# Performance work log

Hardware: AMD Instinct MI355X
Metric: run time of the kernel (lower is better)

The kernel has to match this reference:

```python
import jax, jax.numpy as jnp
import numpy as np

B, F, N = 16, 128, 20000  # batch, feature (edge==node==message size), num nodes
M = F  # message_size = edge_feature_size


def setup_inputs() -> dict:
    key = jax.random.key(0)
    ks = jax.random.split(key, 9)
    s = 1.0 / np.sqrt(F)
    return {
        "h_w": jax.random.normal(ks[0], (B, F, N), jnp.float32),
        "h_v": jax.random.normal(ks[1], (B, F), jnp.float32),
        "e_wv": jax.random.normal(ks[2], (B, F, N), jnp.float32),
        "W_e2m": jax.random.normal(ks[3], (M, F), jnp.float32) * s,
        "b_e2m": jax.random.normal(ks[4], (M,), jnp.float32) * s,
        "W_n2m": jax.random.normal(ks[5], (M, F), jnp.float32) * s,
        "b_n2m": jax.random.normal(ks[6], (M,), jnp.float32) * s,
        "W_resize": jax.random.normal(ks[7], (M, 3 * M), jnp.float32) * (1.0 / np.sqrt(3 * M)),
        "b_resize": jax.random.normal(ks[8], (M,), jnp.float32) * (1.0 / np.sqrt(3 * M)),
    }


def reference(h_w, h_v, e_wv, W_e2m, b_e2m, W_n2m, b_n2m, W_resize, b_resize):
    # Per-node loop vectorized over the node axis n.
    # tmp_msg = cat([e2m(e_wv[:,:,n]), n2m(h_w[:,:,n]), n2m(h_v)], dim=1)
    # message[:,:,n] = resize_m(tmp_msg)
    # Split W_resize into its three column blocks to avoid materializing the
    # [B, 3M, N] concat: resize(cat(a,b,c)) = Wa@a + Wb@b + Wc@c + b.
    Wa = W_resize[:, :M]          # acts on e2m output
    Wb = W_resize[:, M:2 * M]     # acts on n2m(h_w)
    Wc = W_resize[:, 2 * M:]      # acts on n2m(h_v)

    em = jnp.einsum('bfn,mf->bmn', e_wv, W_e2m) + b_e2m[:, None]   # [B,M,N]
    nw = jnp.einsum('bfn,mf->bmn', h_w, W_n2m) + b_n2m[:, None]    # [B,M,N]
    nv = h_v @ W_n2m.T + b_n2m                                      # [B,M]

    msg = (jnp.einsum('bmn,km->bkn', em, Wa)
           + jnp.einsum('bmn,km->bkn', nw, Wb)
           + ((nv @ Wc.T) + b_resize)[:, :, None])                  # [B,M,N]
    return msg
```

## Files before the change

kernel.cpp:

```cpp
#include <hip/hip_runtime.h>
#include <hip/hip_bf16.h>

typedef __attribute__((ext_vector_type(8))) short bf16x8;
typedef __attribute__((ext_vector_type(4))) float f32x4;

#define B_DIM 16
#define F_DIM 128
#define N_DIM 20000
#define M_DIM 128
#define NW 32
#define NSUB 2
#define TILES_PER_B 625
#define NBLK (16 * TILES_PER_B)
#define MAT_LDS (NW * 128)

static __device__ inline unsigned short f2bf(float x) {
    union { float f; unsigned u; } v; v.f = x;
    unsigned r = v.u + 0x7fffu + ((v.u >> 16) & 1u);
    return (unsigned short)(r >> 16);
}

__global__ __launch_bounds__(256) void precompute_mats(
    const float* __restrict__ W_rs,
    const float* __restrict__ W_e2m,
    const float* __restrict__ W_n2m,
    unsigned short* __restrict__ wsA,
    unsigned short* __restrict__ wsB)
{
    int idx = blockIdx.x * 256 + threadIdx.x;
    int k = idx >> 7;
    int f = idx & 127;
    float a = 0.f, b = 0.f;
    for (int m = 0; m < 128; ++m) {
        a += W_rs[k * 384 + m]       * W_e2m[m * 128 + f];
        b += W_rs[k * 384 + 128 + m] * W_n2m[m * 128 + f];
    }
    int mt = k >> 4, row = k & 15;
    int c = f >> 5, kk = f & 31;
    int lane = ((kk >> 3) << 4) | row;
    int j = kk & 7;
    int off = ((mt * 4 + c) * 64 + lane) * 8 + j;
    wsA[off] = f2bf(a);
    wsB[off] = f2bf(b);
}

__global__ __launch_bounds__(128) void precompute_bias(
    const float* __restrict__ W_rs,
    const float* __restrict__ h_v,
    const float* __restrict__ b_e2m,
    const float* __restrict__ b_n2m,
    const float* __restrict__ b_rs,
    const float* __restrict__ W_n2m,
    float* __restrict__ bias)
{
    __shared__ float nv_s[128];
    int b = blockIdx.x;
    int t = threadIdx.x;
    {
        float nv = b_n2m[t];
        for (int f = 0; f < 128; ++f)
            nv += h_v[b * 128 + f] * W_n2m[t * 128 + f];
        nv_s[t] = nv;
    }
    __syncthreads();
    {
        float acc = b_rs[t];
        for (int m = 0; m < 128; ++m) {
            acc += W_rs[t * 384 + m]       * b_e2m[m];
            acc += W_rs[t * 384 + 128 + m] * b_n2m[m];
            acc += W_rs[t * 384 + 256 + m] * nv_s[m];
        }
        bias[b * 128 + t] = acc;
    }
}

__global__ __launch_bounds__(256, 6) void msg_main(
    const float* __restrict__ e_wv,
    const float* __restrict__ h_w,
    const unsigned short* __restrict__ wsA,
    const unsigned short* __restrict__ wsB,
    const float* __restrict__ bias,
    float* __restrict__ out)
{
    __shared__ unsigned short lds[2 * MAT_LDS];

    int tid = threadIdx.x;
    int w   = tid >> 6;
    int l   = tid & 63;
    int blk0 = blockIdx.x;
    int blk  = (blk0 & 7) * (NBLK / 8) + (blk0 >> 3);
    int b   = blk / TILES_PER_B;
    int n0  = (blk - b * TILES_PER_B) * NW;

    const float* eb = e_wv + (size_t)b * (F_DIM * (size_t)N_DIM) + n0;
    const float* wb = h_w  + (size_t)b * (F_DIM * (size_t)N_DIM) + n0;

    int nq = l & 7;
    int fp0 = 0 * 32 + w * 8 + (l >> 3);
    int fp1 = 1 * 32 + w * 8 + (l >> 3);
    f32x4 ve[2][2], vw[2][2];
    ve[0][0] = *(const f32x4*)(eb + (size_t)(2 * fp0)     * N_DIM + 4 * nq);
    ve[0][1] = *(const f32x4*)(eb + (size_t)(2 * fp0 + 1) * N_DIM + 4 * nq);
    ve[1][0] = *(const f32x4*)(eb + (size_t)(2 * fp1)     * N_DIM + 4 * nq);
    ve[1][1] = *(const f32x4*)(eb + (size_t)(2 * fp1 + 1) * N_DIM + 4 * nq);
    vw[0][0] = *(const f32x4*)(wb + (size_t)(2 * fp0)     * N_DIM + 4 * nq);
    vw[0][1] = *(const f32x4*)(wb + (size_t)(2 * fp0 + 1) * N_DIM + 4 * nq);
    vw[1][0] = *(const f32x4*)(wb + (size_t)(2 * fp1)     * N_DIM + 4 * nq);
    vw[1][1] = *(const f32x4*)(wb + (size_t)(2 * fp1 + 1) * N_DIM + 4 * nq);

    char* ldsc = (char*)lds;
#pragma unroll
    for (int u = 0; u < 2; ++u) {
        int fp = u ? fp1 : fp0;
#pragma unroll
        for (int q = 0; q < 4; ++q) {
            int nn = 4 * nq + q;
            unsigned fo = (unsigned)(fp * 4) ^ (unsigned)((nn & 7) << 4);
            unsigned off = (unsigned)(nn * 256) + fo;
            unsigned pe = (unsigned)f2bf(ve[u][0][q]) | ((unsigned)f2bf(ve[u][1][q]) << 16);
            unsigned pw = (unsigned)f2bf(vw[u][0][q]) | ((unsigned)f2bf(vw[u][1][q]) << 16);
            *(unsigned*)(ldsc + off) = pe;
            *(unsigned*)(ldsc + 2 * MAT_LDS + off) = pw;
        }
    }
    __syncthreads();

    int ln = l & 15, g = l >> 4;
    f32x4 acc[2][NSUB];
#pragma unroll
    for (int mtL = 0; mtL < 2; ++mtL)
#pragma unroll
        for (int ns = 0; ns < NSUB; ++ns) acc[mtL][ns] = (f32x4)(0.f);

    const bf16x8* Af = (const bf16x8*)wsA;
    const bf16x8* Bf = (const bf16x8*)wsB;
    const char* ldse = ldsc;
    const char* ldsw = ldsc + 2 * MAT_LDS;
    unsigned rbase = (unsigned)(ln * 256);
    unsigned rx = (unsigned)((ln & 7) << 4);

#pragma unroll
    for (int c = 0; c < 4; ++c) {
        bf16x8 a0 = Af[((2 * w + 0) * 4 + c) * 64 + l];
        bf16x8 a1 = Af[((2 * w + 1) * 4 + c) * 64 + l];
        bf16x8 b0 = Bf[((2 * w + 0) * 4 + c) * 64 + l];
        bf16x8 b1 = Bf[((2 * w + 1) * 4 + c) * 64 + l];
        unsigned fbyte = (unsigned)((c * 32 + g * 8) * 2) ^ rx;
#pragma unroll
        for (int ns = 0; ns < NSUB; ++ns) {
            bf16x8 xe = *(const bf16x8*)(ldse + ns * 4096 + rbase + fbyte);
            bf16x8 xw = *(const bf16x8*)(ldsw + ns * 4096 + rbase + fbyte);
            acc[0][ns] = __builtin_amdgcn_mfma_f32_16x16x32_bf16(a0, xe, acc[0][ns], 0, 0, 0);
            acc[0][ns] = __builtin_amdgcn_mfma_f32_16x16x32_bf16(b0, xw, acc[0][ns], 0, 0, 0);
            acc[1][ns] = __builtin_amdgcn_mfma_f32_16x16x32_bf16(a1, xe, acc[1][ns], 0, 0, 0);
            acc[1][ns] = __builtin_amdgcn_mfma_f32_16x16x32_bf16(b1, xw, acc[1][ns], 0, 0, 0);
        }
    }

    const f32x4* bias4 = (const f32x4*)(bias + b * 128);
    float* O = out + (size_t)b * (M_DIM * (size_t)N_DIM) + n0 + ln;
#pragma unroll
    for (int mtL = 0; mtL < 2; ++mtL) {
        int mt = 2 * w + mtL;
        f32x4 bb = bias4[mt * 4 + g];
#pragma unroll
        for (int ns = 0; ns < NSUB; ++ns) {
#pragma unroll
            for (int r = 0; r < 4; ++r) {
                int k = mt * 16 + g * 4 + r;
                __builtin_nontemporal_store(acc[mtL][ns][r] + bb[r],
                                            O + (size_t)k * N_DIM + ns * 16);
            }
        }
    }
}

extern "C" void kernel_launch(void* const* d_in, const int* in_sizes, int n_in,
                              void* d_out, int out_size, void* d_ws, size_t ws_size,
                              hipStream_t stream) {
    const float* h_w   = (const float*)d_in[0];
    const float* h_v   = (const float*)d_in[1];
    const float* e_wv  = (const float*)d_in[2];
    const float* W_e2m = (const float*)d_in[3];
    const float* b_e2m = (const float*)d_in[4];
    const float* W_n2m = (const float*)d_in[5];
    const float* b_n2m = (const float*)d_in[6];
    const float* W_rs  = (const float*)d_in[7];
    const float* b_rs  = (const float*)d_in[8];
    float* out = (float*)d_out;

    unsigned short* wsA = (unsigned short*)d_ws;
    unsigned short* wsB = wsA + 128 * 128;
    float* bias = (float*)((char*)d_ws + 65536);

    precompute_mats<<<64, 256, 0, stream>>>(W_rs, W_e2m, W_n2m, wsA, wsB);
    precompute_bias<<<16, 128, 0, stream>>>(W_rs, h_v, b_e2m, b_n2m, b_rs, W_n2m, bias);
    msg_main<<<NBLK, 256, 0, stream>>>(e_wv, h_w, wsA, wsB, bias, out);
}
```

Before: 150.1 us.

## Stage fp32 inputs via global_load_lds then convert to bf16 in LDS

After: 139.7 us. 1.07x faster.

```diff
diff --git a/kernel.cpp b/kernel.cpp
--- a/kernel.cpp
+++ b/kernel.cpp
@@ -12,7 +12,12 @@
 #define NSUB 2
 #define TILES_PER_B 625
 #define NBLK (16 * TILES_PER_B)
-#define MAT_LDS (NW * 128)
+#define LDS_F32_MAT 16384
+#define LDS_BF16_OFF 32768
+#define LDS_BF16_MAT 8192
+
+#define AS1 __attribute__((address_space(1)))
+#define AS3 __attribute__((address_space(3)))
 
 static __device__ inline unsigned short f2bf(float x) {
     union { float f; unsigned u; } v; v.f = x;
@@ -74,7 +79,7 @@
     }
 }
 
-__global__ __launch_bounds__(256, 6) void msg_main(
+__global__ __launch_bounds__(256) void msg_main(
     const float* __restrict__ e_wv,
     const float* __restrict__ h_w,
     const unsigned short* __restrict__ wsA,
@@ -82,7 +87,7 @@
     const float* __restrict__ bias,
     float* __restrict__ out)
 {
-    __shared__ unsigned short lds[2 * MAT_LDS];
+    __shared__ __align__(16) unsigned char smem[49152];
 
     int tid = threadIdx.x;
     int w   = tid >> 6;
@@ -95,32 +100,44 @@
     const float* eb = e_wv + (size_t)b * (F_DIM * (size_t)N_DIM) + n0;
     const float* wb = h_w  + (size_t)b * (F_DIM * (size_t)N_DIM) + n0;
 
-    int nq = l & 7;
-    int fp0 = 0 * 32 + w * 8 + (l >> 3);
-    int fp1 = 1 * 32 + w * 8 + (l >> 3);
-    f32x4 ve[2][2], vw[2][2];
-    ve[0][0] = *(const f32x4*)(eb + (size_t)(2 * fp0)     * N_DIM + 4 * nq);
-    ve[0][1] = *(const f32x4*)(eb + (size_t)(2 * fp0 + 1) * N_DIM + 4 * nq);
-    ve[1][0] = *(const f32x4*)(eb + (size_t)(2 * fp1)     * N_DIM + 4 * nq);
-    ve[1][1] = *(const f32x4*)(eb + (size_t)(2 * fp1 + 1) * N_DIM + 4 * nq);
-    vw[0][0] = *(const f32x4*)(wb + (size_t)(2 * fp0)     * N_DIM + 4 * nq);
-    vw[0][1] = *(const f32x4*)(wb + (size_t)(2 * fp0 + 1) * N_DIM + 4 * nq);
-    vw[1][0] = *(const f32x4*)(wb + (size_t)(2 * fp1)     * N_DIM + 4 * nq);
-    vw[1][1] = *(const f32x4*)(wb + (size_t)(2 * fp1 + 1) * N_DIM + 4 * nq);
-
-    char* ldsc = (char*)lds;
-#pragma unroll
-    for (int u = 0; u < 2; ++u) {
-        int fp = u ? fp1 : fp0;
-#pragma unroll
-        for (int q = 0; q < 4; ++q) {
-            int nn = 4 * nq + q;
-            unsigned fo = (unsigned)(fp * 4) ^ (unsigned)((nn & 7) << 4);
-            unsigned off = (unsigned)(nn * 256) + fo;
-            unsigned pe = (unsigned)f2bf(ve[u][0][q]) | ((unsigned)f2bf(ve[u][1][q]) << 16);
-            unsigned pw = (unsigned)f2bf(vw[u][0][q]) | ((unsigned)f2bf(vw[u][1][q]) << 16);
-            *(unsigned*)(ldsc + off) = pe;
-            *(unsigned*)(ldsc + 2 * MAT_LDS + off) = pw;
+    {
+        int qsw = ((l & 7) ^ (l >> 3)) * 4;
+        int fl  = l >> 3;
+#pragma unroll
+        for (int i = 0; i < 4; ++i) {
+            int f_base = i * 32 + w * 8;
+            unsigned char* ld_e = smem + f_base * 128;
+            unsigned char* ld_w = smem + LDS_F32_MAT + f_base * 128;
+            const float* ge = eb + (size_t)(f_base + fl) * N_DIM + qsw;
+            const float* gw = wb + (size_t)(f_base + fl) * N_DIM + qsw;
+            __builtin_amdgcn_global_load_lds((const AS1 unsigned*)ge, (AS3 unsigned*)ld_e, 16, 0, 0);
+            __builtin_amdgcn_global_load_lds((const AS1 unsigned*)gw, (AS3 unsigned*)ld_w, 16, 0, 0);
+        }
+    }
+    __syncthreads();
+
+    {
+        int m    = tid >> 7;
+        int u    = tid & 127;
+        int fp   = u >> 1;
+        int half = u & 1;
+        const unsigned char* fsrc = smem + m * LDS_F32_MAT;
+        unsigned char* bdst = smem + LDS_BF16_OFF + m * LDS_BF16_MAT;
+        int f0 = 2 * fp, f1 = 2 * fp + 1;
+        int x0 = f0 & 7, x1 = f1 & 7;
+#pragma unroll
+        for (int j = 0; j < 4; ++j) {
+            int q = half * 4 + j;
+            f32x4 a = *(const f32x4*)(fsrc + f0 * 128 + (q ^ x0) * 16);
+            f32x4 c = *(const f32x4*)(fsrc + f1 * 128 + (q ^ x1) * 16);
+#pragma unroll
+            for (int e = 0; e < 4; ++e) {
+                int n = q * 4 + e;
+                unsigned pk = (unsigned)f2bf(a[e]) | ((unsigned)f2bf(c[e]) << 16);
+                unsigned off = (unsigned)(n * 256) +
+                               ((unsigned)(fp * 4) ^ (unsigned)((n & 7) << 4));
+                *(unsigned*)(bdst + off) = pk;
+            }
         }
     }
     __syncthreads();
@@ -134,8 +151,8 @@
 
     const bf16x8* Af = (const bf16x8*)wsA;
     const bf16x8* Bf = (const bf16x8*)wsB;
-    const char* ldse = ldsc;
-    const char* ldsw = ldsc + 2 * MAT_LDS;
+    const unsigned char* ldse = smem + LDS_BF16_OFF;
+    const unsigned char* ldsw = smem + LDS_BF16_OFF + LDS_BF16_MAT;
     unsigned rbase = (unsigned)(ln * 256);
     unsigned rx = (unsigned)((ln & 7) << 4);
 
@@ -168,8 +185,7 @@
 #pragma unroll
             for (int r = 0; r < 4; ++r) {
                 int k = mt * 16 + g * 4 + r;
-                __builtin_nontemporal_store(acc[mtL][ns][r] + bb[r],
-                                            O + (size_t)k * N_DIM + ns * 16);
+                O[(size_t)k * N_DIM + ns * 16] = acc[mtL][ns][r] + bb[r];
             }
         }
     }
```
